# Performance work log

Hardware: AMD Instinct MI355X
Metric: run time of the kernel (lower is better)

Reference implementation:

```python
import jax, jax.numpy as jnp
import numpy as np

N, E, D, H, L, T = 50000, 200000, 128, 64, 2, 4
SIB_ID = 1
EPS = 1e-6


def _log_map_zero(x, c):
    # x: [N, D+1] on hyperboloid of curvature c; returns [N, D] tangent at origin.
    sqrt_c = jnp.sqrt(c)
    x0 = jnp.clip(sqrt_c * x[..., 0], 1.0 + 1e-7, None)
    dist = jnp.arccosh(x0) / sqrt_c                      # [N]
    sp = x[..., 1:]                                      # [N, D]
    nrm = jnp.maximum(jnp.linalg.norm(sp, axis=-1), EPS)
    return sp * (dist / nrm)[..., None]


def _exp_map_zero(v, c):
    # v: [N, D] tangent at origin; returns [N, D+1] on hyperboloid.
    sqrt_c = jnp.sqrt(c)
    nrm = jnp.maximum(jnp.linalg.norm(v, axis=-1), EPS)  # [N]
    th = sqrt_c * nrm
    x0 = jnp.cosh(th) / sqrt_c
    sp = v * (jnp.sinh(th) / (sqrt_c * nrm))[..., None]
    return jnp.concatenate([x0[..., None], sp], axis=-1)


def setup_inputs() -> dict:
    key = jax.random.key(0)
    ks = jax.random.split(key, 12)
    v0 = 0.1 * jax.random.normal(ks[0], (N, D), dtype=jnp.float32)
    x_hyp = _exp_map_zero(v0, 1.0)
    edge_index = jax.random.randint(ks[1], (2, E), 0, N, dtype=jnp.int32)
    edge_types = jax.random.randint(ks[2], (E,), 0, T, dtype=jnp.int32)
    edge_weights = jax.random.uniform(ks[3], (E,), dtype=jnp.float32) + 0.1
    s_lin = 1.0 / np.sqrt(D)
    s_w1 = 1.0 / np.sqrt(3 * D)
    s_w2 = 1.0 / np.sqrt(H)
    return {
        "x_hyp": x_hyp,
        "edge_index": edge_index,
        "edge_types": edge_types,
        "edge_weights": edge_weights,
        "lin_w": s_lin * jax.random.normal(ks[4], (L, D, D), dtype=jnp.float32),
        "lin_b": jnp.zeros((L, D), dtype=jnp.float32),
        "ln_g": jnp.ones((L, D), dtype=jnp.float32),
        "ln_b": jnp.zeros((L, D), dtype=jnp.float32),
        "edge_emb": 0.02 * jax.random.normal(ks[5], (L, T, D), dtype=jnp.float32),
        "attn_w1": s_w1 * jax.random.normal(ks[6], (L, 3 * D, H), dtype=jnp.float32),
        "attn_b1": jnp.zeros((L, H), dtype=jnp.float32),
        "attn_w2": s_w2 * jax.random.normal(ks[7], (L, H, 1), dtype=jnp.float32),
        "attn_b2": jnp.zeros((L, 1), dtype=jnp.float32),
        "sibling_boost": jnp.full((L,), 0.15, dtype=jnp.float32),
        "curvature": jnp.ones((L,), dtype=jnp.float32),
    }


def _layer(x_hyp, edge_index, edge_types, edge_weights,
           lin_w, lin_b, ln_g, ln_b, emb, w1, b1, w2, b2, sib, curv):
    n = x_hyp.shape[0]
    # curvature is read via .item() in the original -> detached constant
    c = jax.lax.stop_gradient(jnp.clip(curv, 0.1, 10.0))
    x_tan = _log_map_zero(x_hyp, c)                      # [N, D]
    x_lin = x_tan @ lin_w.T + lin_b                      # [N, D]
    src, dst = edge_index[0], edge_index[1]              # PyG: x_j=src, x_i=dst
    x_i = x_lin[dst]                                     # [E, D]
    x_j = x_lin[src]                                     # [E, D]
    e_emb = emb[edge_types]                              # [E, D]
    attn_in = jnp.concatenate([x_i, x_j, e_emb], axis=-1)  # [E, 3D]
    h = jax.nn.silu(attn_in @ w1 + b1)                   # [E, H]
    score = (h @ w2 + b2)[..., 0]                        # [E]
    score = score + jnp.log(jnp.clip(edge_weights, EPS, None))
    score = score + (edge_types == SIB_ID).astype(score.dtype) * sib
    # segment softmax over destination nodes
    seg_max = jax.ops.segment_max(score, dst, num_segments=n)
    ex = jnp.exp(score - seg_max[dst])
    seg_sum = jax.ops.segment_sum(ex, dst, num_segments=n)
    alpha = ex / (seg_sum[dst] + 1e-16)                  # [E]
    msg = (x_j + e_emb) * (alpha * edge_weights)[:, None]  # [E, D]
    x_agg = jax.ops.segment_sum(msg, dst, num_segments=n)  # [N, D]
    x_out = x_tan + x_agg                                # dropout is identity in eval
    mu = jnp.mean(x_out, axis=-1, keepdims=True)
    var = jnp.var(x_out, axis=-1, keepdims=True)
    x_out = (x_out - mu) * jax.lax.rsqrt(var + 1e-5) * ln_g + ln_b
    return _exp_map_zero(x_out, c)


def reference(x_hyp, edge_index, edge_types, edge_weights, lin_w, lin_b,
              ln_g, ln_b, edge_emb, attn_w1, attn_b1, attn_w2, attn_b2,
              sibling_boost, curvature):
    for i in range(lin_w.shape[0]):
        x_hyp = _layer(x_hyp, edge_index, edge_types, edge_weights,
                       lin_w[i], lin_b[i], ln_g[i], ln_b[i], edge_emb[i],
                       attn_w1[i], attn_b1[i], attn_w2[i], attn_b2[i],
                       sibling_boost[i], curvature[i])
    return x_hyp
```

## Files before the change

kernel.cpp:

```cpp
#include <hip/hip_runtime.h>
#include <math.h>

#define WAVE 64
#define KMAX 32

typedef __attribute__((ext_vector_type(8))) short bf16x8;
typedef __attribute__((ext_vector_type(4))) float f32x4;

__device__ __forceinline__ unsigned short f2b(float f) {
    unsigned u = __float_as_uint(f);
    unsigned r = (u + 0x7FFFu + ((u >> 16) & 1u)) >> 16;
    return (unsigned short)r;
}
__device__ __forceinline__ float b2f(unsigned short u) {
    return __uint_as_float(((unsigned)u) << 16);
}
__device__ __forceinline__ float frcp(float x)   { return __builtin_amdgcn_rcpf(x); }
__device__ __forceinline__ float frsq(float x)   { return __builtin_amdgcn_rsqf(x); }
__device__ __forceinline__ float fsqrt2(float x) { return __builtin_amdgcn_sqrtf(x); }
__device__ __forceinline__ float silu(float x)   { return x * frcp(1.f + __expf(-x)); }
__device__ __forceinline__ float facosh(float x) { return __logf(x + fsqrt2(x * x - 1.f)); }

__device__ __forceinline__ void dual_gemm_16(
    unsigned short* sm,
    const unsigned short* __restrict__ LW, const unsigned short* __restrict__ WT,
    const float* __restrict__ bias,
    unsigned short* __restrict__ xlin, unsigned short* __restrict__ acat,
    int base, int N, int tid)
{
    int wave = tid >> 6;
    int lane = tid & 63;
    int quad = lane >> 4;
    int l16  = lane & 15;
    int nloc = tid >> 4;

    __syncthreads();

    bf16x8 a[4];
    #pragma unroll
    for (int kk = 0; kk < 4; ++kk)
        a[kk] = *(const bf16x8*)&sm[l16 * 136 + kk * 32 + quad * 8];

    f32x4 acc[2];
    acc[0] = (f32x4){0.f, 0.f, 0.f, 0.f};
    acc[1] = (f32x4){0.f, 0.f, 0.f, 0.f};
    #pragma unroll
    for (int kk = 0; kk < 4; ++kk) {
        #pragma unroll
        for (int t = 0; t < 2; ++t) {
            int nt = wave * 2 + t;
            bf16x8 b = *(const bf16x8*)&LW[(size_t)(nt * 16 + l16) * 128 + kk * 32 + quad * 8];
            acc[t] = __builtin_amdgcn_mfma_f32_16x16x32_bf16(a[kk], b, acc[t], 0, 0, 0);
        }
    }
    __syncthreads();
    #pragma unroll
    for (int t = 0; t < 2; ++t) {
        int nt = wave * 2 + t;
        float bv = bias[nt * 16 + l16];
        #pragma unroll
        for (int r = 0; r < 4; ++r)
            sm[(quad * 4 + r) * 136 + nt * 16 + l16] = f2b(acc[t][r] + bv);
    }
    __syncthreads();

    bf16x8 a2[4];
    #pragma unroll
    for (int kk = 0; kk < 4; ++kk)
        a2[kk] = *(const bf16x8*)&sm[l16 * 136 + kk * 32 + quad * 8];
    int node = base + nloc;
    if (node < N)
        *(bf16x8*)&xlin[(size_t)node * 128 + 8 * l16] =
            *(const bf16x8*)&sm[nloc * 136 + 8 * l16];

    f32x4 acc2[2];
    acc2[0] = (f32x4){0.f, 0.f, 0.f, 0.f};
    acc2[1] = (f32x4){0.f, 0.f, 0.f, 0.f};
    #pragma unroll
    for (int kk = 0; kk < 4; ++kk) {
        #pragma unroll
        for (int t = 0; t < 2; ++t) {
            int nt = wave * 2 + t;
            bf16x8 b = *(const bf16x8*)&WT[(size_t)(nt * 16 + l16) * 128 + kk * 32 + quad * 8];
            acc2[t] = __builtin_amdgcn_mfma_f32_16x16x32_bf16(a2[kk], b, acc2[t], 0, 0, 0);
        }
    }
    #pragma unroll
    for (int t = 0; t < 2; ++t) {
        int nt = wave * 2 + t;
        #pragma unroll
        for (int r = 0; r < 4; ++r) {
            int rr = base + quad * 4 + r;
            if (rr < N) acat[(size_t)rr * 128 + nt * 16 + l16] = f2b(acc2[t][r]);
        }
    }
}

__global__ __launch_bounds__(256) void k_pre(
    const float* __restrict__ lin_w, const float* __restrict__ w1,
    const float* __restrict__ b1, const float* __restrict__ emb,
    unsigned short* __restrict__ lw_bf, unsigned short* __restrict__ Wt_bf,
    float* __restrict__ ae, int* __restrict__ deg, int N, int PB)
{
    int bid = blockIdx.x, tid = threadIdx.x;
    if (bid < PB) {
        int l = bid / 129, bx = bid % 129;
        const float* lwl = lin_w + (size_t)l * 16384;
        const float* w1l = w1 + (size_t)l * 384 * 64;
        if (bx < 64) {
            int idx = bx * 256 + tid;
            lw_bf[l * 16384 + idx] = f2b(lwl[idx]);
        } else if (bx < 128) {
            int idx = (bx - 64) * 256 + tid;
            int o = idx >> 7, i = idx & 127;
            float v = (o < 64) ? w1l[i * 64 + o] : w1l[(128 + i) * 64 + (o - 64)];
            Wt_bf[l * 16384 + idx] = f2b(v);
        } else {
            int t = tid >> 6, h = tid & 63;
            float s = b1[l * 64 + h];
            #pragma unroll 8
            for (int i = 0; i < 128; ++i)
                s += emb[l * 512 + t * 128 + i] * w1l[(256 + i) * 64 + h];
            ae[l * 256 + tid] = s;
        }
    } else {
        int i0 = ((bid - PB) * 256 + tid) * 4;
        if (i0 + 3 < N) {
            *(int4*)&deg[i0] = make_int4(0, 0, 0, 0);
        } else {
            #pragma unroll
            for (int k2 = 0; k2 < 4; ++k2)
                if (i0 + k2 < N) deg[i0 + k2] = 0;
        }
    }
}

__global__ __launch_bounds__(256) void k_main(
    const int* __restrict__ ei, const int* __restrict__ et,
    const float* __restrict__ ew, const float* __restrict__ xh,
    const float* __restrict__ curv,
    const unsigned short* __restrict__ LW, const unsigned short* __restrict__ WT,
    const float* __restrict__ lb,
    int* __restrict__ deg, int2* __restrict__ epack,
    unsigned short* __restrict__ xtan_bf,
    unsigned short* __restrict__ xlin, unsigned short* __restrict__ acat,
    int E, int N, int ECH)
{
    __shared__ __align__(16) unsigned short sm[16 * 136];
    int bid = blockIdx.x, tid = threadIdx.x;
    if (bid < ECH) {
        int e = bid * 256 + tid;
        if (e < E) {
            int dst = ei[E + e];
            int rank = atomicAdd(&deg[dst], 1);
            if (rank < KMAX) {
                int2 r;
                r.x = ei[e] | (et[e] << 24);
                r.y = __float_as_int(ew[e]);
                epack[(size_t)dst * KMAX + rank] = r;
            }
        }
        return;
    }
    int base = (bid - ECH) * 16;
    int l16  = tid & 15;
    int nloc = tid >> 4;
    int node = base + nloc;
    int nodec = node < N ? node : N - 1;

    float c = fminf(fmaxf(curv[0], 0.1f), 10.f);
    float sqc = fsqrt2(c);
    const float* row = xh + (size_t)nodec * 129;
    float x0 = row[0];
    float v[8];
    #pragma unroll
    for (int j = 0; j < 8; ++j) v[j] = row[1 + 8 * l16 + j];
    float n2 = 0.f;
    #pragma unroll
    for (int j = 0; j < 8; ++j) n2 += v[j] * v[j];
    #pragma unroll
    for (int m = 1; m < 16; m <<= 1) n2 += __shfl_xor(n2, m, WAVE);
    float nrm = fmaxf(fsqrt2(n2), 1e-6f);
    float x0c = fmaxf(sqc * x0, 1.f + 1e-7f);
    float f = facosh(x0c) * frcp(sqc) * frcp(nrm);

    bf16x8 o8;
    #pragma unroll
    for (int j = 0; j < 8; ++j) o8[j] = (short)f2b(v[j] * f);
    if (node < N)
        *(bf16x8*)&xtan_bf[(size_t)node * 128 + 8 * l16] = o8;
    *(bf16x8*)&sm[nloc * 136 + 8 * l16] = o8;

    dual_gemm_16(sm, LW, WT, lb, xlin, acat, base, N, tid);
}

__global__ __launch_bounds__(256) void k_B(
    const int* __restrict__ deg, const int2* __restrict__ epack,
    const unsigned short* __restrict__ acat, const unsigned short* __restrict__ xlin,
    unsigned short* __restrict__ xtan_bf, const float* __restrict__ ae,
    const float* __restrict__ emb, const float* __restrict__ w2,
    const float* __restrict__ b2, const float* __restrict__ sib,
    const float* __restrict__ g, const float* __restrict__ b,
    const float* __restrict__ curv, const float* __restrict__ curv_n,
    int last, float* __restrict__ out, int N,
    const unsigned short* __restrict__ LWn, const unsigned short* __restrict__ WTn,
    const float* __restrict__ lbn,
    unsigned short* __restrict__ xlin_o, unsigned short* __restrict__ acat_o)
{
    __shared__ __align__(16) unsigned short sm[16 * 136];
    int tid = threadIdx.x;
    int lane = tid & 63;
    int quad = lane >> 4;
    int l16  = lane & 15;
    int gw = (blockIdx.x * 256 + tid) >> 6;
    int wid = gw * 4 + quad;
    bool nv = wid < N;
    int widc = nv ? wid : N - 1;

    float c = fminf(fmaxf(curv[0], 0.1f), 10.f);
    float sqc = fsqrt2(c);
    float rsqc = frcp(sqc);
    int dg = deg[widc];
    dg = dg < KMAX ? dg : KMAX;
    int p0 = widc * KMAX;
    int p1 = nv ? p0 + dg : p0;

    ushort4 adu = *(const ushort4*)&acat[(size_t)widc * 128 + 4 * l16];
    float ad0 = b2f(adu.x), ad1 = b2f(adu.y), ad2 = b2f(adu.z), ad3 = b2f(adu.w);
    float4 w2v = *(const float4*)&w2[4 * l16];
    float b2v = b2[0], sibv = sib[0];

    float acc[8];
    #pragma unroll
    for (int j = 0; j < 8; ++j) acc[j] = 0.f;
    float S = 0.f;
    float4 St = make_float4(0.f, 0.f, 0.f, 0.f);

    for (int j = 0; ; ++j) {
        int p = p0 + j;
        bool ev = p < p1;
        if (!__any(ev)) break;
        int2 r = epack[ev ? p : 0];
        int src = r.x & 0xFFFFFF;
        int t = ((unsigned)r.x) >> 24;
        float w = __int_as_float(r.y);

        ushort4 asu = *(const ushort4*)&acat[(size_t)src * 128 + 64 + 4 * l16];
        float4 av = *(const float4*)&ae[t * 64 + 4 * l16];
        float d = silu(ad0 + b2f(asu.x) + av.x) * w2v.x
                + silu(ad1 + b2f(asu.y) + av.y) * w2v.y
                + silu(ad2 + b2f(asu.z) + av.z) * w2v.z
                + silu(ad3 + b2f(asu.w) + av.w) * w2v.w;
        #pragma unroll
        for (int m = 1; m < 16; m <<= 1) d += __shfl_xor(d, m, WAVE);
        float s = d + b2v + __logf(fmaxf(w, 1e-6f));
        if (t == 1) s += sibv;
        float exv = ev ? __expf(s) : 0.f;
        S += exv;
        float cf = exv * w;

        bf16x8 xu = *(const bf16x8*)&xlin[(size_t)src * 128 + 8 * l16];
        #pragma unroll
        for (int k = 0; k < 8; ++k)
            acc[k] += b2f((unsigned short)xu[k]) * cf;
        St.x += (t == 0) ? cf : 0.f;
        St.y += (t == 1) ? cf : 0.f;
        St.z += (t == 2) ? cf : 0.f;
        St.w += (t == 3) ? cf : 0.f;
    }

    #pragma unroll
    for (int tt = 0; tt < 4; ++tt) {
        float stv = (tt == 0) ? St.x : (tt == 1) ? St.y : (tt == 2) ? St.z : St.w;
        float4 em0 = *(const float4*)&emb[tt * 128 + 8 * l16];
        float4 em1 = *(const float4*)&emb[tt * 128 + 8 * l16 + 4];
        acc[0] += em0.x * stv; acc[1] += em0.y * stv;
        acc[2] += em0.z * stv; acc[3] += em0.w * stv;
        acc[4] += em1.x * stv; acc[5] += em1.y * stv;
        acc[6] += em1.z * stv; acc[7] += em1.w * stv;
    }

    float inv = frcp(S + 1e-16f);
    bf16x8 xtu = *(const bf16x8*)&xtan_bf[(size_t)widc * 128 + 8 * l16];
    float y[8];
    #pragma unroll
    for (int j = 0; j < 8; ++j)
        y[j] = b2f((unsigned short)xtu[j]) + acc[j] * inv;

    float sum = 0.f, sq = 0.f;
    #pragma unroll
    for (int j = 0; j < 8; ++j) { sum += y[j]; sq += y[j] * y[j]; }
    #pragma unroll
    for (int m = 1; m < 16; m <<= 1) {
        sum += __shfl_xor(sum, m, WAVE);
        sq  += __shfl_xor(sq, m, WAVE);
    }
    float mu = sum * (1.f / 128.f);
    float var = sq * (1.f / 128.f) - mu * mu;
    float invs = frsq(var + 1e-5f);
    float4 g0 = *(const float4*)&g[8 * l16];
    float4 g1 = *(const float4*)&g[8 * l16 + 4];
    float4 bb0 = *(const float4*)&b[8 * l16];
    float4 bb1 = *(const float4*)&b[8 * l16 + 4];
    y[0] = (y[0] - mu) * invs * g0.x + bb0.x;
    y[1] = (y[1] - mu) * invs * g0.y + bb0.y;
    y[2] = (y[2] - mu) * invs * g0.z + bb0.z;
    y[3] = (y[3] - mu) * invs * g0.w + bb0.w;
    y[4] = (y[4] - mu) * invs * g1.x + bb1.x;
    y[5] = (y[5] - mu) * invs * g1.y + bb1.y;
    y[6] = (y[6] - mu) * invs * g1.z + bb1.z;
    y[7] = (y[7] - mu) * invs * g1.w + bb1.w;

    float nrm2 = 0.f;
    #pragma unroll
    for (int j = 0; j < 8; ++j) nrm2 += y[j] * y[j];
    #pragma unroll
    for (int m = 1; m < 16; m <<= 1) nrm2 += __shfl_xor(nrm2, m, WAVE);
    float nrm = fmaxf(fsqrt2(nrm2), 1e-6f);
    float th = sqc * nrm;
    float e = __expf(th);
    float einv = frcp(e);
    float ch = 0.5f * (e + einv);
    float sh = 0.5f * (e - einv);
    float sc = sh * frcp(sqc * nrm);

    if (last) {
        if (nv) {
            float* o = out + (size_t)wid * 129;
            if (l16 == 0) o[0] = ch * rsqc;
            #pragma unroll
            for (int j = 0; j < 8; ++j) o[1 + 8 * l16 + j] = y[j] * sc;
        }
    } else {
        float x0 = ch * rsqc;
        float c2 = fminf(fmaxf(curv_n[0], 0.1f), 10.f);
        float sqc2 = fsqrt2(c2);
        float x0c = fmaxf(sqc2 * x0, 1.f + 1e-7f);
        float dist = facosh(x0c) * frcp(sqc2);
        float nsp = fmaxf(sh * rsqc, 1e-6f);
        float sf = sc * dist * frcp(nsp);
        bf16x8 o8;
        #pragma unroll
        for (int j = 0; j < 8; ++j) o8[j] = (short)f2b(y[j] * sf);
        if (nv)
            *(bf16x8*)&xtan_bf[(size_t)wid * 128 + 8 * l16] = o8;
        *(bf16x8*)&sm[(tid >> 4) * 136 + 8 * l16] = o8;
        dual_gemm_16(sm, LWn, WTn, lbn, xlin_o, acat_o, blockIdx.x * 16, N, tid);
    }
}

extern "C" void kernel_launch(void* const* d_in, const int* in_sizes, int n_in,
                              void* d_out, int out_size, void* d_ws, size_t ws_size,
                              hipStream_t stream) {
    const float* x_hyp = (const float*)d_in[0];
    const int*   ei    = (const int*)d_in[1];
    const int*   et    = (const int*)d_in[2];
    const float* ew    = (const float*)d_in[3];
    const float* lin_w = (const float*)d_in[4];
    const float* lin_b = (const float*)d_in[5];
    const float* ln_g  = (const float*)d_in[6];
    const float* ln_b  = (const float*)d_in[7];
    const float* emb   = (const float*)d_in[8];
    const float* w1    = (const float*)d_in[9];
    const float* b1    = (const float*)d_in[10];
    const float* w2    = (const float*)d_in[11];
    const float* b2    = (const float*)d_in[12];
    const float* sib   = (const float*)d_in[13];
    const float* curv  = (const float*)d_in[14];
    float* out = (float*)d_out;

    const int N = in_sizes[0] / 129;
    const int E = in_sizes[2];
    const int L = in_sizes[4] / (128 * 128);
    const int ECH = (E + 255) / 256;
    const int NB16 = (N + 15) / 16;
    const int PB = L * 129;
    const int ZB = (N + 1023) / 1024;

    unsigned short* xtan_bf = (unsigned short*)d_ws;
    unsigned short* xlin0 = xtan_bf + (size_t)N * 128;
    unsigned short* acat0 = xlin0 + (size_t)N * 128;
    unsigned short* xlin1 = acat0 + (size_t)N * 128;
    unsigned short* acat1 = xlin1 + (size_t)N * 128;
    int2* epack = (int2*)(acat1 + (size_t)N * 128);
    unsigned short* lw_bf = (unsigned short*)(epack + (size_t)N * KMAX);
    unsigned short* Wt_bf = lw_bf + (size_t)L * 16384;
    float* ae   = (float*)(Wt_bf + (size_t)L * 16384);
    int* deg    = (int*)(ae + (size_t)L * 256);

    k_pre<<<PB + ZB, 256, 0, stream>>>(lin_w, w1, b1, emb,
                                       lw_bf, Wt_bf, ae, deg, N, PB);

    k_main<<<ECH + NB16, 256, 0, stream>>>(
        ei, et, ew, x_hyp, curv, lw_bf, Wt_bf, lin_b,
        deg, epack, xtan_bf, xlin0, acat0, E, N, ECH);

    for (int l = 0; l < L; ++l) {
        int ln = (l + 1 < L) ? l + 1 : l;
        unsigned short* xin = (l & 1) ? xlin1 : xlin0;
        unsigned short* ain = (l & 1) ? acat1 : acat0;
        unsigned short* xot = (l & 1) ? xlin0 : xlin1;
        unsigned short* aot = (l & 1) ? acat0 : acat1;
        k_B<<<NB16, 256, 0, stream>>>(
            deg, epack, ain, xin, xtan_bf,
            ae + (size_t)l * 256, emb + (size_t)l * 512,
            w2 + (size_t)l * 64, b2 + l, sib + l,
            ln_g + (size_t)l * 128, ln_b + (size_t)l * 128,
            curv + l, curv + ln,
            l == L - 1 ? 1 : 0, out, N,
            lw_bf + (size_t)ln * 16384, Wt_bf + (size_t)ln * 16384,
            lin_b + (size_t)ln * 128, xot, aot);
    }
}
```

Baseline: 222.5 us.

## Prefetch next edge's gathers and broadcast edge list via shuffles in aggregation kernel

Each 16-lane group now loads its whole padded edge list (32 entries) in one vectorized load and hands entries to lanes with shuffles, instead of a dependent global load per iteration. Gathers for the next edge (source activations, edge-type embedding, xlin row) are issued before the current edge is processed, forming a software pipeline. Per-node loads such as xtan and acat are hoisted to the kernel start. This hides gather latency at the cost of more live registers, which may lower occupancy.

```diff
diff --git a/kernel.cpp b/kernel.cpp
--- a/kernel.cpp
+++ b/kernel.cpp
@@ -217,17 +217,20 @@
     bool nv = wid < N;
     int widc = nv ? wid : N - 1;
 
+    int dg = deg[widc];
+    const int4* bp = (const int4*)(epack + widc * KMAX);
+    int4 myent = bp[l16];
+    bf16x8 xtu = *(const bf16x8*)&xtan_bf[(size_t)widc * 128 + 8 * l16];
+    ushort4 adu = *(const ushort4*)&acat[(size_t)widc * 128 + 4 * l16];
+    float4 w2v = *(const float4*)&w2[4 * l16];
+
     float c = fminf(fmaxf(curv[0], 0.1f), 10.f);
     float sqc = fsqrt2(c);
     float rsqc = frcp(sqc);
-    int dg = deg[widc];
     dg = dg < KMAX ? dg : KMAX;
-    int p0 = widc * KMAX;
-    int p1 = nv ? p0 + dg : p0;
-
-    ushort4 adu = *(const ushort4*)&acat[(size_t)widc * 128 + 4 * l16];
+    dg = nv ? dg : 0;
+
     float ad0 = b2f(adu.x), ad1 = b2f(adu.y), ad2 = b2f(adu.z), ad3 = b2f(adu.w);
-    float4 w2v = *(const float4*)&w2[4 * l16];
     float b2v = b2[0], sibv = sib[0];
 
     float acc[8];
@@ -236,17 +239,33 @@
     float S = 0.f;
     float4 St = make_float4(0.f, 0.f, 0.f, 0.f);
 
-    for (int j = 0; ; ++j) {
-        int p = p0 + j;
-        bool ev = p < p1;
-        if (!__any(ev)) break;
-        int2 r = epack[ev ? p : 0];
-        int src = r.x & 0xFFFFFF;
-        int t = ((unsigned)r.x) >> 24;
-        float w = __int_as_float(r.y);
-
-        ushort4 asu = *(const ushort4*)&acat[(size_t)src * 128 + 64 + 4 * l16];
-        float4 av = *(const float4*)&ae[t * 64 + 4 * l16];
+    int jmax = dg;
+    jmax = max(jmax, __shfl_xor(jmax, 16, WAVE));
+    jmax = max(jmax, __shfl_xor(jmax, 32, WAVE));
+
+    ushort4 asu_n; bf16x8 xu_n; float4 av_n;
+    float w_n = 1.f; int t_n = 0; bool ev_n = false;
+
+#define FETCH(J) {                                                          \
+        int lsrc = (quad << 4) + ((J) >> 1);                                \
+        int rx = __shfl(((J) & 1) ? myent.z : myent.x, lsrc, WAVE);         \
+        int ry = __shfl(((J) & 1) ? myent.w : myent.y, lsrc, WAVE);         \
+        ev_n = (J) < dg;                                                    \
+        int src = ev_n ? (rx & 0xFFFFFF) : 0;                               \
+        t_n = ev_n ? (int)(((unsigned)rx) >> 24) : 0;                       \
+        float wv = __int_as_float(ry);                                      \
+        w_n = ev_n ? wv : 1.f;                                              \
+        asu_n = *(const ushort4*)&acat[(size_t)src * 128 + 64 + 4 * l16];   \
+        av_n  = *(const float4*)&ae[t_n * 64 + 4 * l16];                    \
+        xu_n  = *(const bf16x8*)&xlin[(size_t)src * 128 + 8 * l16];         \
+    }
+
+    if (jmax > 0) FETCH(0);
+    for (int j = 0; j < jmax; ++j) {
+        ushort4 asu = asu_n; bf16x8 xu = xu_n; float4 av = av_n;
+        float w = w_n; int t = t_n; bool ev = ev_n;
+        if (j + 1 < jmax) FETCH(j + 1);
+
         float d = silu(ad0 + b2f(asu.x) + av.x) * w2v.x
                 + silu(ad1 + b2f(asu.y) + av.y) * w2v.y
                 + silu(ad2 + b2f(asu.z) + av.z) * w2v.z
@@ -259,7 +278,6 @@
         S += exv;
         float cf = exv * w;
 
-        bf16x8 xu = *(const bf16x8*)&xlin[(size_t)src * 128 + 8 * l16];
         #pragma unroll
         for (int k = 0; k < 8; ++k)
             acc[k] += b2f((unsigned short)xu[k]) * cf;
@@ -268,6 +286,7 @@
         St.z += (t == 2) ? cf : 0.f;
         St.w += (t == 3) ? cf : 0.f;
     }
+#undef FETCH
 
     #pragma unroll
     for (int tt = 0; tt < 4; ++tt) {
@@ -281,7 +300,6 @@
     }
 
     float inv = frcp(S + 1e-16f);
-    bf16x8 xtu = *(const bf16x8*)&xtan_bf[(size_t)widc * 128 + 8 * l16];
     float y[8];
     #pragma unroll
     for (int j = 0; j < 8; ++j)
```

Measured after the change: 222.8 us. About the same (+0.1%).

## Prefetch edge bucket and software-pipeline two edges per iteration in k_B

Applied to the files above, without the earlier changes.

The aggregation kernel now loads each node's whole 32-entry edge bucket once with a vector load and broadcasts entries through lane shuffles. It handles two edges per iteration and prefetches the next pair's gathers while computing the current pair, so the serial gather latency is hidden. The residual tangent buffer is also stored in fp32 instead of bf16, which doubles its traffic in exchange for accuracy, and the per-node loads are hoisted to the top of the kernel. The extra prefetch registers may reduce occupancy.

```diff
diff --git a/kernel.cpp b/kernel.cpp
--- a/kernel.cpp
+++ b/kernel.cpp
@@ -142,7 +142,7 @@
     const unsigned short* __restrict__ LW, const unsigned short* __restrict__ WT,
     const float* __restrict__ lb,
     int* __restrict__ deg, int2* __restrict__ epack,
-    unsigned short* __restrict__ xtan_bf,
+    float* __restrict__ xtf,
     unsigned short* __restrict__ xlin, unsigned short* __restrict__ acat,
     int E, int N, int ECH)
 {
@@ -184,11 +184,17 @@
     float x0c = fmaxf(sqc * x0, 1.f + 1e-7f);
     float f = facosh(x0c) * frcp(sqc) * frcp(nrm);
 
+    float vf[8];
     bf16x8 o8;
     #pragma unroll
-    for (int j = 0; j < 8; ++j) o8[j] = (short)f2b(v[j] * f);
-    if (node < N)
-        *(bf16x8*)&xtan_bf[(size_t)node * 128 + 8 * l16] = o8;
+    for (int j = 0; j < 8; ++j) {
+        vf[j] = v[j] * f;
+        o8[j] = (short)f2b(vf[j]);
+    }
+    if (node < N) {
+        *(float4*)&xtf[(size_t)node * 128 + 8 * l16]     = make_float4(vf[0], vf[1], vf[2], vf[3]);
+        *(float4*)&xtf[(size_t)node * 128 + 8 * l16 + 4] = make_float4(vf[4], vf[5], vf[6], vf[7]);
+    }
     *(bf16x8*)&sm[nloc * 136 + 8 * l16] = o8;
 
     dual_gemm_16(sm, LW, WT, lb, xlin, acat, base, N, tid);
@@ -197,7 +203,7 @@
 __global__ __launch_bounds__(256) void k_B(
     const int* __restrict__ deg, const int2* __restrict__ epack,
     const unsigned short* __restrict__ acat, const unsigned short* __restrict__ xlin,
-    unsigned short* __restrict__ xtan_bf, const float* __restrict__ ae,
+    float* __restrict__ xtf, const float* __restrict__ ae,
     const float* __restrict__ emb, const float* __restrict__ w2,
     const float* __restrict__ b2, const float* __restrict__ sib,
     const float* __restrict__ g, const float* __restrict__ b,
@@ -217,17 +223,21 @@
     bool nv = wid < N;
     int widc = nv ? wid : N - 1;
 
+    int dg = deg[widc];
+    const int4* bp = (const int4*)(epack + (size_t)widc * KMAX);
+    int4 myent = bp[l16];
+    float4 xt0 = *(const float4*)&xtf[(size_t)widc * 128 + 8 * l16];
+    float4 xt1 = *(const float4*)&xtf[(size_t)widc * 128 + 8 * l16 + 4];
+    ushort4 adu = *(const ushort4*)&acat[(size_t)widc * 128 + 4 * l16];
+    float4 w2v = *(const float4*)&w2[4 * l16];
+
     float c = fminf(fmaxf(curv[0], 0.1f), 10.f);
     float sqc = fsqrt2(c);
     float rsqc = frcp(sqc);
-    int dg = deg[widc];
     dg = dg < KMAX ? dg : KMAX;
-    int p0 = widc * KMAX;
-    int p1 = nv ? p0 + dg : p0;
-
-    ushort4 adu = *(const ushort4*)&acat[(size_t)widc * 128 + 4 * l16];
+    dg = nv ? dg : 0;
+
     float ad0 = b2f(adu.x), ad1 = b2f(adu.y), ad2 = b2f(adu.z), ad3 = b2f(adu.w);
-    float4 w2v = *(const float4*)&w2[4 * l16];
     float b2v = b2[0], sibv = sib[0];
 
     float acc[8];
@@ -236,38 +246,88 @@
     float S = 0.f;
     float4 St = make_float4(0.f, 0.f, 0.f, 0.f);
 
-    for (int j = 0; ; ++j) {
-        int p = p0 + j;
-        bool ev = p < p1;
-        if (!__any(ev)) break;
-        int2 r = epack[ev ? p : 0];
-        int src = r.x & 0xFFFFFF;
-        int t = ((unsigned)r.x) >> 24;
-        float w = __int_as_float(r.y);
-
-        ushort4 asu = *(const ushort4*)&acat[(size_t)src * 128 + 64 + 4 * l16];
-        float4 av = *(const float4*)&ae[t * 64 + 4 * l16];
-        float d = silu(ad0 + b2f(asu.x) + av.x) * w2v.x
-                + silu(ad1 + b2f(asu.y) + av.y) * w2v.y
-                + silu(ad2 + b2f(asu.z) + av.z) * w2v.z
-                + silu(ad3 + b2f(asu.w) + av.w) * w2v.w;
-        #pragma unroll
-        for (int m = 1; m < 16; m <<= 1) d += __shfl_xor(d, m, WAVE);
-        float s = d + b2v + __logf(fmaxf(w, 1e-6f));
-        if (t == 1) s += sibv;
-        float exv = ev ? __expf(s) : 0.f;
-        S += exv;
-        float cf = exv * w;
-
-        bf16x8 xu = *(const bf16x8*)&xlin[(size_t)src * 128 + 8 * l16];
+    int jm = dg;
+    jm = max(jm, __shfl_xor(jm, 16, WAVE));
+    jm = max(jm, __shfl_xor(jm, 32, WAVE));
+    int jmax = (jm + 1) >> 1;
+
+    ushort4 asuA_n, asuB_n; bf16x8 xuA_n, xuB_n; float4 avA_n, avB_n;
+    float wA_n = 1.f, wB_n = 1.f; int tA_n = 0, tB_n = 0;
+    bool eA_n = false, eB_n = false;
+
+#define FETCHP(J) {                                                           \
+        int lsrc = (quad << 4) + (J);                                         \
+        int r0x = __shfl(myent.x, lsrc, WAVE);                                \
+        int r0y = __shfl(myent.y, lsrc, WAVE);                                \
+        int r1x = __shfl(myent.z, lsrc, WAVE);                                \
+        int r1y = __shfl(myent.w, lsrc, WAVE);                                \
+        eA_n = (2 * (J)) < dg;                                                \
+        eB_n = (2 * (J) + 1) < dg;                                            \
+        int sA = eA_n ? (r0x & 0xFFFFFF) : 0;                                 \
+        int sB = eB_n ? (r1x & 0xFFFFFF) : 0;                                 \
+        tA_n = eA_n ? (int)(((unsigned)r0x) >> 24) : 0;                       \
+        tB_n = eB_n ? (int)(((unsigned)r1x) >> 24) : 0;                       \
+        wA_n = eA_n ? __int_as_float(r0y) : 1.f;                              \
+        wB_n = eB_n ? __int_as_float(r1y) : 1.f;                              \
+        asuA_n = *(const ushort4*)&acat[(size_t)sA * 128 + 64 + 4 * l16];     \
+        asuB_n = *(const ushort4*)&acat[(size_t)sB * 128 + 64 + 4 * l16];     \
+        avA_n  = *(const float4*)&ae[tA_n * 64 + 4 * l16];                    \
+        avB_n  = *(const float4*)&ae[tB_n * 64 + 4 * l16];                    \
+        xuA_n  = *(const bf16x8*)&xlin[(size_t)sA * 128 + 8 * l16];           \
+        xuB_n  = *(const bf16x8*)&xlin[(size_t)sB * 128 + 8 * l16];           \
+    }
+
+    if (jmax > 0) FETCHP(0);
+    for (int j = 0; j < jmax; ++j) {
+        ushort4 asuA = asuA_n, asuB = asuB_n;
+        bf16x8 xuA = xuA_n, xuB = xuB_n;
+        float4 avA = avA_n, avB = avB_n;
+        float wA = wA_n, wB = wB_n;
+        int tA = tA_n, tB = tB_n;
+        bool eA = eA_n, eB = eB_n;
+        if (j + 1 < jmax) FETCHP(j + 1);
+
+        float dA = silu(ad0 + b2f(asuA.x) + avA.x) * w2v.x
+                 + silu(ad1 + b2f(asuA.y) + avA.y) * w2v.y
+                 + silu(ad2 + b2f(asuA.z) + avA.z) * w2v.z
+                 + silu(ad3 + b2f(asuA.w) + avA.w) * w2v.w;
+        float dB = silu(ad0 + b2f(asuB.x) + avB.x) * w2v.x
+                 + silu(ad1 + b2f(asuB.y) + avB.y) * w2v.y
+                 + silu(ad2 + b2f(asuB.z) + avB.z) * w2v.z
+                 + silu(ad3 + b2f(asuB.w) + avB.w) * w2v.w;
+        #pragma unroll
+        for (int m = 1; m < 16; m <<= 1) {
+            dA += __shfl_xor(dA, m, WAVE);
+            dB += __shfl_xor(dB, m, WAVE);
+        }
+        float sA = dA + b2v + __logf(fmaxf(wA, 1e-6f));
+        if (tA == 1) sA += sibv;
+        float exA = eA ? __expf(sA) : 0.f;
+        S += exA;
+        float cfA = exA * wA;
+
+        float sB2 = dB + b2v + __logf(fmaxf(wB, 1e-6f));
+        if (tB == 1) sB2 += sibv;
+        float exB = eB ? __expf(sB2) : 0.f;
+        S += exB;
+        float cfB = exB * wB;
+
         #pragma unroll
         for (int k = 0; k < 8; ++k)
-            acc[k] += b2f((unsigned short)xu[k]) * cf;
-        St.x += (t == 0) ? cf : 0.f;
-        St.y += (t == 1) ? cf : 0.f;
-        St.z += (t == 2) ? cf : 0.f;
-        St.w += (t == 3) ? cf : 0.f;
-    }
+            acc[k] += b2f((unsigned short)xuA[k]) * cfA;
+        #pragma unroll
+        for (int k = 0; k < 8; ++k)
+            acc[k] += b2f((unsigned short)xuB[k]) * cfB;
+        St.x += (tA == 0) ? cfA : 0.f;
+        St.y += (tA == 1) ? cfA : 0.f;
+        St.z += (tA == 2) ? cfA : 0.f;
+        St.w += (tA == 3) ? cfA : 0.f;
+        St.x += (tB == 0) ? cfB : 0.f;
+        St.y += (tB == 1) ? cfB : 0.f;
+        St.z += (tB == 2) ? cfB : 0.f;
+        St.w += (tB == 3) ? cfB : 0.f;
+    }
+#undef FETCHP
 
     #pragma unroll
     for (int tt = 0; tt < 4; ++tt) {
@@ -281,11 +341,15 @@
     }
 
     float inv = frcp(S + 1e-16f);
-    bf16x8 xtu = *(const bf16x8*)&xtan_bf[(size_t)widc * 128 + 8 * l16];
     float y[8];
-    #pragma unroll
-    for (int j = 0; j < 8; ++j)
-        y[j] = b2f((unsigned short)xtu[j]) + acc[j] * inv;
+    y[0] = xt0.x + acc[0] * inv;
+    y[1] = xt0.y + acc[1] * inv;
+    y[2] = xt0.z + acc[2] * inv;
+    y[3] = xt0.w + acc[3] * inv;
+    y[4] = xt1.x + acc[4] * inv;
+    y[5] = xt1.y + acc[5] * inv;
+    y[6] = xt1.z + acc[6] * inv;
+    y[7] = xt1.w + acc[7] * inv;
 
     float sum = 0.f, sq = 0.f;
     #pragma unroll
@@ -339,11 +403,17 @@
         float dist = facosh(x0c) * frcp(sqc2);
         float nsp = fmaxf(sh * rsqc, 1e-6f);
         float sf = sc * dist * frcp(nsp);
+        float tf[8];
         bf16x8 o8;
         #pragma unroll
-        for (int j = 0; j < 8; ++j) o8[j] = (short)f2b(y[j] * sf);
-        if (nv)
-            *(bf16x8*)&xtan_bf[(size_t)wid * 128 + 8 * l16] = o8;
+        for (int j = 0; j < 8; ++j) {
+            tf[j] = y[j] * sf;
+            o8[j] = (short)f2b(tf[j]);
+        }
+        if (nv) {
+            *(float4*)&xtf[(size_t)wid * 128 + 8 * l16]     = make_float4(tf[0], tf[1], tf[2], tf[3]);
+            *(float4*)&xtf[(size_t)wid * 128 + 8 * l16 + 4] = make_float4(tf[4], tf[5], tf[6], tf[7]);
+        }
         *(bf16x8*)&sm[(tid >> 4) * 136 + 8 * l16] = o8;
         dual_gemm_16(sm, LWn, WTn, lbn, xlin_o, acat_o, blockIdx.x * 16, N, tid);
     }
@@ -377,8 +447,8 @@
     const int PB = L * 129;
     const int ZB = (N + 1023) / 1024;
 
-    unsigned short* xtan_bf = (unsigned short*)d_ws;
-    unsigned short* xlin0 = xtan_bf + (size_t)N * 128;
+    float* xtf = (float*)d_ws;
+    unsigned short* xlin0 = (unsigned short*)(xtf + (size_t)N * 128);
     unsigned short* acat0 = xlin0 + (size_t)N * 128;
     unsigned short* xlin1 = acat0 + (size_t)N * 128;
     unsigned short* acat1 = xlin1 + (size_t)N * 128;
@@ -393,7 +463,7 @@
 
     k_main<<<ECH + NB16, 256, 0, stream>>>(
         ei, et, ew, x_hyp, curv, lw_bf, Wt_bf, lin_b,
-        deg, epack, xtan_bf, xlin0, acat0, E, N, ECH);
+        deg, epack, xtf, xlin0, acat0, E, N, ECH);
 
     for (int l = 0; l < L; ++l) {
         int ln = (l + 1 < L) ? l + 1 : l;
@@ -402,7 +472,7 @@
         unsigned short* xot = (l & 1) ? xlin0 : xlin1;
         unsigned short* aot = (l & 1) ? acat0 : acat1;
         k_B<<<NB16, 256, 0, stream>>>(
-            deg, epack, ain, xin, xtan_bf,
+            deg, epack, ain, xin, xtf,
             ae + (size_t)l * 256, emb + (size_t)l * 512,
             w2 + (size_t)l * 64, b2 + l, sib + l,
             ln_g + (size_t)l * 128, ln_b + (size_t)l * 128,
```

Result: no change. 222.5 us (+0.0%).
